# Kernel tuning notes

Measured on AMD Instinct MI355X. Metric: run time of the kernel, lower is better.

The kernel has to match this reference:

```python
import jax, jax.numpy as jnp
import numpy as np

D_MODEL = 1024
N_HEAD = 16
D_K = D_MODEL // N_HEAD
NEG = -1e9


def setup_inputs() -> dict:
    key = jax.random.key(0)
    ks = jax.random.split(key, 9)
    B, S = 2, 2048
    scale = 1.0 / np.sqrt(D_MODEL)
    x = jax.random.normal(ks[0], (B, S, D_MODEL), dtype=jnp.float32)
    mask = jnp.tril(jnp.ones((S, S), dtype=jnp.int32))  # causal: 0 => masked
    Wq = jax.random.normal(ks[1], (D_MODEL, D_MODEL), dtype=jnp.float32) * scale
    bq = jnp.zeros((D_MODEL,), dtype=jnp.float32)
    Wk = jax.random.normal(ks[2], (D_MODEL, D_MODEL), dtype=jnp.float32) * scale
    bk = jnp.zeros((D_MODEL,), dtype=jnp.float32)
    Wv = jax.random.normal(ks[3], (D_MODEL, D_MODEL), dtype=jnp.float32) * scale
    bv = jnp.zeros((D_MODEL,), dtype=jnp.float32)
    Wo = jax.random.normal(ks[4], (D_MODEL, D_MODEL), dtype=jnp.float32) * scale
    bo = jnp.zeros((D_MODEL,), dtype=jnp.float32)
    return {"x": x, "mask": mask, "Wq": Wq, "bq": bq, "Wk": Wk, "bk": bk,
            "Wv": Wv, "bv": bv, "Wo": Wo, "bo": bo}


def reference(x, mask, Wq, bq, Wk, bk, Wv, bv, Wo, bo):
    B, S, _ = x.shape
    # torch Linear: y = x @ W.T + b
    def split_heads(y):  # [B,S,D] -> [B,H,S,d_k]
        return y.reshape(B, S, N_HEAD, D_K).transpose(0, 2, 1, 3)
    Q = split_heads(x @ Wq.T + bq)
    K = split_heads(x @ Wk.T + bk)
    V = split_heads(x @ Wv.T + bv)
    scores = jnp.einsum('bhqd,bhkd->bhqk', Q, K) / jnp.sqrt(jnp.float32(D_K))
    scores = jnp.where(mask[None, None, :, :] == 0, jnp.float32(NEG), scores)
    attn = jax.nn.softmax(scores, axis=-1)
    out = jnp.einsum('bhqk,bhkd->bhqd', attn, V)
    out = out.transpose(0, 2, 1, 3).reshape(B, S, D_MODEL)
    return out @ Wo.T + bo
```

## Files before the change

### kernel.cpp

```cpp
#include <hip/hip_runtime.h>
#include <hip/hip_bf16.h>
#include <stdint.h>

#define DM    1024
#define NHEAD 16
#define DKH   64
#define SEQ   2048
#define NB    2
#define MTOT  (NB*SEQ)
#define LSTR  72
#define QSCL  0.18033688f

typedef __hip_bfloat16 bf16;
typedef __attribute__((ext_vector_type(8))) short bf16x8;
typedef __attribute__((ext_vector_type(4))) short bf16x4;
typedef __attribute__((ext_vector_type(4))) float f32x4;

#define MFMA16(a,b,c) __builtin_amdgcn_mfma_f32_16x16x32_bf16((a),(b),(c),0,0,0)

#if __has_builtin(__builtin_amdgcn_exp2f)
#define EXP2F(x) __builtin_amdgcn_exp2f(x)
#else
#define EXP2F(x) __expf(0.69314718056f * (x))
#endif

__device__ __forceinline__ void async_copy16(const void* g, void* l) {
  __builtin_amdgcn_global_load_lds((const __attribute__((address_space(1))) uint32_t*)g,
                                   (__attribute__((address_space(3))) uint32_t*)l,
                                   16, 0, 0);
}

__device__ __forceinline__ short f32_bf16_bits(float f) {
  uint32_t u = __builtin_bit_cast(uint32_t, f);
  u += 0x7FFFu + ((u >> 16) & 1u);
  return (short)(u >> 16);
}

__global__ __launch_bounds__(256) void k_cvt_all(
    const float* __restrict__ x,  const float* __restrict__ Wq,
    const float* __restrict__ Wk, const float* __restrict__ Wv,
    const float* __restrict__ Wo,
    bf16* __restrict__ xb,  bf16* __restrict__ Wqb, bf16* __restrict__ Wkb,
    bf16* __restrict__ Wvb, bf16* __restrict__ Wob) {
  const int NX = (MTOT*DM)/4;
  const int NW = (DM*DM)/4;
  int i = blockIdx.x * 256 + threadIdx.x;
  const float* s; bf16* d; int j; float scl = 1.0f;
  if (i < NX) { s = x; d = xb; j = i; }
  else {
    int t = i - NX;
    int k = t >> 18;
    j = t & (NW - 1);
    s = (k == 0) ? Wq : (k == 1) ? Wk : (k == 2) ? Wv : Wo;
    d = (k == 0) ? Wqb : (k == 1) ? Wkb : (k == 2) ? Wvb : Wob;
    if (k == 0) scl = QSCL;
  }
  float4 v = ((const float4*)s)[j];
  bf16x4 o;
  o[0] = f32_bf16_bits(v.x * scl);
  o[1] = f32_bf16_bits(v.y * scl);
  o[2] = f32_bf16_bits(v.z * scl);
  o[3] = f32_bf16_bits(v.w * scl);
  ((bf16x4*)d)[j] = o;
}

__global__ __launch_bounds__(256) void k_gemm_qkv(
    const bf16* __restrict__ x,
    const bf16* __restrict__ Wq, const bf16* __restrict__ Wk, const bf16* __restrict__ Wv,
    const float* __restrict__ bq, const float* __restrict__ bk, const float* __restrict__ bv,
    bf16* __restrict__ Q, bf16* __restrict__ K, bf16* __restrict__ V) {
  const int id  = blockIdx.x + (blockIdx.y << 5) + (blockIdx.z << 8);
  const int xcd = id & 7;
  const int jj  = id >> 3;
  const int bxi = (xcd << 2) | (jj & 3);
  const int rem = jj >> 2;
  const int byi = rem & 7;
  const int bzi = rem >> 3;

  const bf16* W; const float* bias; bf16* C; float bs;
  if (bzi == 0)      { W = Wq; bias = bq; C = Q; bs = QSCL; }
  else if (bzi == 1) { W = Wk; bias = bk; C = K; bs = 1.0f; }
  else               { W = Wv; bias = bv; C = V; bs = 1.0f; }

  __shared__ __align__(16) short As[128*32];
  __shared__ __align__(16) short Bs[128*32];
  const int tid  = threadIdx.x;
  const int lane = tid & 63;
  const int w    = tid >> 6;
  const int wm   = (w & 1) << 6;
  const int wn   = (w >> 1) << 6;
  const int bm   = bxi << 7;
  const int bn   = byi << 7;
  const int m16  = lane & 15;
  const int quad = lane >> 4;
  const int koff = quad << 3;
  const int c0   = (w << 7) | lane;

  f32x4 acc[4][4] = {};

  for (int k0 = 0; k0 < DM; k0 += 32) {
    __syncthreads();
#pragma unroll
    for (int it = 0; it < 2; ++it) {
      int c   = c0 + (it << 6);
      int row = c >> 2;
      int kc  = c & 3;
      async_copy16(x + (size_t)(bm + row) * DM + k0 + (kc << 3),
                   &As[(size_t)((w << 7) + (it << 6)) << 3]);
      async_copy16(W + (size_t)(bn + row) * DM + k0 + (kc << 3),
                   &Bs[(size_t)((w << 7) + (it << 6)) << 3]);
    }
    __syncthreads();

    bf16x8 af[4], bfv[4];
#pragma unroll
    for (int t = 0; t < 4; ++t)
      af[t]  = *(const bf16x8*)&As[(wm + t*16 + m16) * 32 + koff];
#pragma unroll
    for (int t = 0; t < 4; ++t)
      bfv[t] = *(const bf16x8*)&Bs[(wn + t*16 + m16) * 32 + koff];
#pragma unroll
    for (int i = 0; i < 4; ++i)
#pragma unroll
      for (int j = 0; j < 4; ++j)
        acc[i][j] = MFMA16(af[i], bfv[j], acc[i][j]);
  }

  const int crow0 = bm + wm + (quad << 2);
  const int ccol0 = bn + wn + m16;
#pragma unroll
  for (int j = 0; j < 4; ++j) {
    float bv = bias[ccol0 + j*16] * bs;
#pragma unroll
    for (int i = 0; i < 4; ++i)
#pragma unroll
      for (int r = 0; r < 4; ++r)
        C[(size_t)(crow0 + i*16 + r) * DM + ccol0 + j*16] =
            (bf16)(acc[i][j][r] + bv);
  }
}

__global__ __launch_bounds__(256) void k_gemm_o(
    const bf16* __restrict__ A, const bf16* __restrict__ W,
    const float* __restrict__ bias, float* __restrict__ C) {
  const int id  = blockIdx.x + (blockIdx.y << 5);
  const int xcd = id & 7;
  const int jj  = id >> 3;
  const int bxi = (xcd << 2) | (jj & 3);
  const int byi = jj >> 2;

  __shared__ __align__(16) short As[128*32];
  __shared__ __align__(16) short Bs[64*32];
  const int tid  = threadIdx.x;
  const int lane = tid & 63;
  const int w    = tid >> 6;
  const int wm   = (w & 1) << 6;
  const int wn   = (w >> 1) << 5;
  const int bm   = bxi << 7;
  const int bn   = byi << 6;
  const int m16  = lane & 15;
  const int quad = lane >> 4;
  const int koff = quad << 3;
  const int cA   = (w << 7) | lane;
  const int cB   = (w << 6) | lane;

  f32x4 acc[4][2] = {};

  for (int k0 = 0; k0 < DM; k0 += 32) {
    __syncthreads();
#pragma unroll
    for (int it = 0; it < 2; ++it) {
      int c   = cA + (it << 6);
      int row = c >> 2;
      int kc  = c & 3;
      async_copy16(A + (size_t)(bm + row) * DM + k0 + (kc << 3),
                   &As[(size_t)((w << 7) + (it << 6)) << 3]);
    }
    {
      int row = cB >> 2;
      int kc  = cB & 3;
      async_copy16(W + (size_t)(bn + row) * DM + k0 + (kc << 3),
                   &Bs[(size_t)(w << 6) << 3]);
    }
    __syncthreads();

    bf16x8 af[4], bfv[2];
#pragma unroll
    for (int t = 0; t < 4; ++t)
      af[t]  = *(const bf16x8*)&As[(wm + t*16 + m16) * 32 + koff];
#pragma unroll
    for (int t = 0; t < 2; ++t)
      bfv[t] = *(const bf16x8*)&Bs[(wn + t*16 + m16) * 32 + koff];
#pragma unroll
    for (int i = 0; i < 4; ++i)
#pragma unroll
      for (int j = 0; j < 2; ++j)
        acc[i][j] = MFMA16(af[i], bfv[j], acc[i][j]);
  }

  const int crow0 = bm + wm + (quad << 2);
  const int ccol0 = bn + wn + m16;
#pragma unroll
  for (int j = 0; j < 2; ++j) {
    float bv = bias[ccol0 + j*16];
#pragma unroll
    for (int i = 0; i < 4; ++i)
#pragma unroll
      for (int r = 0; r < 4; ++r)
        C[(size_t)(crow0 + i*16 + r) * DM + ccol0 + j*16] =
            acc[i][j][r] + bv;
  }
}

__global__ __launch_bounds__(256) void k_transpose_v(const bf16* __restrict__ V,
                                                     bf16* __restrict__ Vt) {
  __shared__ __align__(16) short tile[64][LSTR];
  const int tid = threadIdx.x;
  const int s0  = blockIdx.x << 6;
  const int bh  = blockIdx.y;
  const int b   = bh >> 4, h = bh & 15;
#pragma unroll
  for (int it = 0; it < 2; ++it) {
    int c = tid + (it << 8);
    int s = c >> 3, dc = c & 7;
    bf16x8 v = *(const bf16x8*)&V[(size_t)(b*SEQ + s0 + s) * DM + h*DKH + (dc << 3)];
    *(bf16x8*)&tile[s][dc << 3] = v;
  }
  __syncthreads();
#pragma unroll
  for (int it = 0; it < 2; ++it) {
    int c = tid + (it << 8);
    int d = c >> 3, sc = c & 7;
    bf16x8 ov;
#pragma unroll
    for (int i = 0; i < 8; ++i) {
      int p = (sc << 3) + i;
      ov[i] = tile[(p & 3) * 16 + (p >> 2)][d];
    }
    *(bf16x8*)&Vt[((size_t)bh * DKH + d) * SEQ + s0 + (sc << 3)] = ov;
  }
}

__global__ __launch_bounds__(256) void k_attn(const bf16* __restrict__ Q,
                                              const bf16* __restrict__ K,
                                              const bf16* __restrict__ Vt,
                                              bf16* __restrict__ ctx) {
  __shared__ __align__(16) short Ks[64*LSTR];
  __shared__ __align__(16) short Vs[64*LSTR];
  __shared__ __align__(16) short Ps[4][16*LSTR];

  const int tid  = threadIdx.x;
  const int lane = tid & 63;
  const int w    = tid >> 6;
  const int pi   = blockIdx.x;
  const int bh   = blockIdx.y;
  const int b    = bh >> 4, h = bh & 15;
  const int m16  = lane & 15, quad = lane >> 4;
  const int koff = quad << 3;

  const int qt        = (w < 2) ? pi : 63 - pi;
  const int qw        = (qt << 5) + ((w & 1) << 4);
  const int my_ktmax  = qt >> 1;
  const int blk_ktmax = (63 - pi) >> 1;

  const int r0 = tid >> 3, r1 = r0 + 32, c0 = (tid & 7) << 3;

  const bf16* Kb  = K  + (size_t)(b*SEQ) * DM + h*DKH;
  const bf16* Vtb = Vt + (size_t)bh * DKH * SEQ;

  const bf16* Qb = Q + (size_t)(b*SEQ + qw) * DM + h*DKH;
  bf16x8 qf0 = *(const bf16x8*)(Qb + (size_t)m16*DM + koff);
  bf16x8 qf1 = *(const bf16x8*)(Qb + (size_t)m16*DM + 32 + koff);

  f32x4 o[4] = {};
  float ps[4] = {0.f, 0.f, 0.f, 0.f};
  short* Pw = Ps[w];
  const int qg = qw + (quad << 2);

  bf16x8 pk0 = *(const bf16x8*)(Kb  + (size_t)r0*DM + c0);
  bf16x8 pk1 = *(const bf16x8*)(Kb  + (size_t)r1*DM + c0);
  bf16x8 pv0 = *(const bf16x8*)(Vtb + (size_t)r0*SEQ + c0);
  bf16x8 pv1 = *(const bf16x8*)(Vtb + (size_t)r1*SEQ + c0);

  for (int kt = 0; kt <= blk_ktmax; ++kt) {
    __syncthreads();
    *(bf16x8*)&Ks[r0*LSTR + c0] = pk0;
    *(bf16x8*)&Ks[r1*LSTR + c0] = pk1;
    *(bf16x8*)&Vs[r0*LSTR + c0] = pv0;
    *(bf16x8*)&Vs[r1*LSTR + c0] = pv1;
    __syncthreads();

    if (kt < blk_ktmax) {
      const int kn = (kt + 1) << 6;
      pk0 = *(const bf16x8*)(Kb  + (size_t)(kn + r0)*DM + c0);
      pk1 = *(const bf16x8*)(Kb  + (size_t)(kn + r1)*DM + c0);
      pv0 = *(const bf16x8*)(Vtb + (size_t)r0*SEQ + kn + c0);
      pv1 = *(const bf16x8*)(Vtb + (size_t)r1*SEQ + kn + c0);
    }

    if (kt <= my_ktmax) {
      f32x4 sc[4];
#pragma unroll
      for (int st = 0; st < 4; ++st) {
        bf16x8 kf0 = *(const bf16x8*)&Ks[(st*16 + m16)*LSTR + koff];
        bf16x8 kf1 = *(const bf16x8*)&Ks[(st*16 + m16)*LSTR + 32 + koff];
        f32x4 a = {};
        a = MFMA16(qf0, kf0, a);
        a = MFMA16(qf1, kf1, a);
        sc[st] = a;
      }
      const int kk0 = kt << 6;
      if (kt == my_ktmax) {
#pragma unroll
        for (int r = 0; r < 4; ++r) {
          float e[4];
#pragma unroll
          for (int st = 0; st < 4; ++st) {
            float t = EXP2F(sc[st][r]);
            t = (kk0 + st*16 + m16 <= qg + r) ? t : 0.f;
            e[st] = t; ps[r] += t;
          }
          uint32_t lo = (uint16_t)f32_bf16_bits(e[0]) |
                        ((uint32_t)(uint16_t)f32_bf16_bits(e[1]) << 16);
          uint32_t hi = (uint16_t)f32_bf16_bits(e[2]) |
                        ((uint32_t)(uint16_t)f32_bf16_bits(e[3]) << 16);
          *(uint64_t*)&Pw[((quad << 2) + r)*LSTR + (m16 << 2)] =
              (uint64_t)lo | ((uint64_t)hi << 32);
        }
      } else {
#pragma unroll
        for (int r = 0; r < 4; ++r) {
          float e[4];
#pragma unroll
          for (int st = 0; st < 4; ++st) {
            float t = EXP2F(sc[st][r]);
            e[st] = t; ps[r] += t;
          }
          uint32_t lo = (uint16_t)f32_bf16_bits(e[0]) |
                        ((uint32_t)(uint16_t)f32_bf16_bits(e[1]) << 16);
          uint32_t hi = (uint16_t)f32_bf16_bits(e[2]) |
                        ((uint32_t)(uint16_t)f32_bf16_bits(e[3]) << 16);
          *(uint64_t*)&Pw[((quad << 2) + r)*LSTR + (m16 << 2)] =
              (uint64_t)lo | ((uint64_t)hi << 32);
        }
      }
      asm volatile("s_waitcnt lgkmcnt(0)" ::: "memory");
      bf16x8 pa0 = *(const bf16x8*)&Pw[m16*LSTR + koff];
      bf16x8 pa1 = *(const bf16x8*)&Pw[m16*LSTR + 32 + koff];
#pragma unroll
      for (int t = 0; t < 4; ++t) {
        bf16x8 vf0 = *(const bf16x8*)&Vs[(t*16 + m16)*LSTR + koff];
        bf16x8 vf1 = *(const bf16x8*)&Vs[(t*16 + m16)*LSTR + 32 + koff];
        o[t] = MFMA16(pa0, vf0, o[t]);
        o[t] = MFMA16(pa1, vf1, o[t]);
      }
    }
  }

  bf16* Cb = ctx + (size_t)(b*SEQ + qw) * DM + h*DKH;
#pragma unroll
  for (int r = 0; r < 4; ++r) {
    float v = ps[r];
    v += __shfl_xor(v, 1, 64);
    v += __shfl_xor(v, 2, 64);
    v += __shfl_xor(v, 4, 64);
    v += __shfl_xor(v, 8, 64);
    float inv = 1.0f / v;
#pragma unroll
    for (int t = 0; t < 4; ++t)
      Cb[(size_t)((quad << 2) + r) * DM + t*16 + m16] = (bf16)(o[t][r] * inv);
  }
}

extern "C" void kernel_launch(void* const* d_in, const int* in_sizes, int n_in,
                              void* d_out, int out_size, void* d_ws, size_t ws_size,
                              hipStream_t stream) {
  const float* x  = (const float*)d_in[0];
  const float* Wq = (const float*)d_in[2];
  const float* bq = (const float*)d_in[3];
  const float* Wk = (const float*)d_in[4];
  const float* bk = (const float*)d_in[5];
  const float* Wv = (const float*)d_in[6];
  const float* bv = (const float*)d_in[7];
  const float* Wo = (const float*)d_in[8];
  const float* bo = (const float*)d_in[9];
  float* out = (float*)d_out;

  const size_t SZ = (size_t)MTOT * DM;
  const size_t WZ = (size_t)DM * DM;
  bf16* xb  = (bf16*)d_ws;
  bf16* Wqb = xb  + SZ;
  bf16* Wkb = Wqb + WZ;
  bf16* Wvb = Wkb + WZ;
  bf16* Wob = Wvb + WZ;
  bf16* Qb  = Wob + WZ;
  bf16* Kb  = Qb  + SZ;
  bf16* Vb  = Kb  + SZ;
  bf16* Vtb = Vb  + SZ;
  bf16* Cx  = xb;

  k_cvt_all<<<(SZ/4 + 4*(WZ/4))/256, 256, 0, stream>>>(
      x, Wq, Wk, Wv, Wo, xb, Wqb, Wkb, Wvb, Wob);

  k_gemm_qkv<<<dim3(MTOT/128, DM/128, 3), 256, 0, stream>>>(
      xb, Wqb, Wkb, Wvb, bq, bk, bv, Qb, Kb, Vb);
  k_transpose_v<<<dim3(SEQ/64, NB*NHEAD), 256, 0, stream>>>(Vb, Vtb);
  k_attn<<<dim3(32, NB*NHEAD), 256, 0, stream>>>(Qb, Kb, Vtb, Cx);
  k_gemm_o<<<dim3(MTOT/128, DM/64), 256, 0, stream>>>(Cx, Wob, bo, out);
}
```

Measured before the change: 203.0 us.

## Keep softmax probabilities in registers by computing transposed scores and permuting V

Computes S^T (K as the A operand) so each lane holds scores for one query row across keys, packs the exponentials with hardware bf16 pack instructions straight into the A-operand registers for the PV MFMA, and drops the per-wave LDS staging of P. The V transpose kernel permutes key order so the register layout of P matches V's k dimension. The row-sum reduction is rewritten around the new layout, and launch bounds request higher occupancy. This removes LDS writes, the reads back and a wait per tile, at the cost of a subtle layout coupling between kernels and switching bf16 rounding to the hardware convert.

```diff
diff --git a/kernel.cpp b/kernel.cpp
--- a/kernel.cpp
+++ b/kernel.cpp
@@ -15,6 +15,7 @@
 typedef __attribute__((ext_vector_type(8))) short bf16x8;
 typedef __attribute__((ext_vector_type(4))) short bf16x4;
 typedef __attribute__((ext_vector_type(4))) float f32x4;
+typedef __attribute__((ext_vector_type(4))) uint32_t u32x4;
 
 #define MFMA16(a,b,c) __builtin_amdgcn_mfma_f32_16x16x32_bf16((a),(b),(c),0,0,0)
 
@@ -34,6 +35,12 @@
   uint32_t u = __builtin_bit_cast(uint32_t, f);
   u += 0x7FFFu + ((u >> 16) & 1u);
   return (short)(u >> 16);
+}
+
+__device__ __forceinline__ uint32_t cvt_pk_bf16(float a, float b) {
+  uint32_t r;
+  asm("v_cvt_pk_bf16_f32 %0, %1, %2" : "=v"(r) : "v"(a), "v"(b));
+  return r;
 }
 
 __global__ __launch_bounds__(256) void k_cvt_all(
@@ -234,20 +241,22 @@
     bf16x8 ov;
 #pragma unroll
     for (int i = 0; i < 8; ++i) {
-      int p = (sc << 3) + i;
-      ov[i] = tile[(p & 3) * 16 + (p >> 2)][d];
+      int p  = (sc << 3) + i;
+      int r  = p & 3;
+      int st = ((p >> 5) & 1) | (((p >> 2) & 1) << 1);
+      int q2 = (p >> 3) & 3;
+      ov[i] = tile[st*16 + q2*4 + r][d];
     }
     *(bf16x8*)&Vt[((size_t)bh * DKH + d) * SEQ + s0 + (sc << 3)] = ov;
   }
 }
 
-__global__ __launch_bounds__(256) void k_attn(const bf16* __restrict__ Q,
-                                              const bf16* __restrict__ K,
-                                              const bf16* __restrict__ Vt,
-                                              bf16* __restrict__ ctx) {
+__global__ __launch_bounds__(256, 8) void k_attn(const bf16* __restrict__ Q,
+                                                 const bf16* __restrict__ K,
+                                                 const bf16* __restrict__ Vt,
+                                                 bf16* __restrict__ ctx) {
   __shared__ __align__(16) short Ks[64*LSTR];
   __shared__ __align__(16) short Vs[64*LSTR];
-  __shared__ __align__(16) short Ps[4][16*LSTR];
 
   const int tid  = threadIdx.x;
   const int lane = tid & 63;
@@ -273,9 +282,9 @@
   bf16x8 qf1 = *(const bf16x8*)(Qb + (size_t)m16*DM + 32 + koff);
 
   f32x4 o[4] = {};
-  float ps[4] = {0.f, 0.f, 0.f, 0.f};
-  short* Pw = Ps[w];
-  const int qg = qw + (quad << 2);
+  float psum = 0.f;
+  const int qrow  = qw + m16;
+  const int kquad = quad << 2;
 
   bf16x8 pk0 = *(const bf16x8*)(Kb  + (size_t)r0*DM + c0);
   bf16x8 pk1 = *(const bf16x8*)(Kb  + (size_t)r1*DM + c0);
@@ -299,54 +308,52 @@
     }
 
     if (kt <= my_ktmax) {
-      f32x4 sc[4];
-#pragma unroll
-      for (int st = 0; st < 4; ++st) {
-        bf16x8 kf0 = *(const bf16x8*)&Ks[(st*16 + m16)*LSTR + koff];
-        bf16x8 kf1 = *(const bf16x8*)&Ks[(st*16 + m16)*LSTR + 32 + koff];
-        f32x4 a = {};
-        a = MFMA16(qf0, kf0, a);
-        a = MFMA16(qf1, kf1, a);
-        sc[st] = a;
-      }
-      const int kk0 = kt << 6;
+      u32x4 p0, p1;
+      const int kbase = (kt << 6) + kquad;
       if (kt == my_ktmax) {
 #pragma unroll
-        for (int r = 0; r < 4; ++r) {
+        for (int st = 0; st < 4; ++st) {
+          bf16x8 kf0 = *(const bf16x8*)&Ks[(st*16 + m16)*LSTR + koff];
+          bf16x8 kf1 = *(const bf16x8*)&Ks[(st*16 + m16)*LSTR + 32 + koff];
+          f32x4 a = {};
+          a = MFMA16(kf0, qf0, a);
+          a = MFMA16(kf1, qf1, a);
           float e[4];
 #pragma unroll
-          for (int st = 0; st < 4; ++st) {
-            float t = EXP2F(sc[st][r]);
-            t = (kk0 + st*16 + m16 <= qg + r) ? t : 0.f;
-            e[st] = t; ps[r] += t;
+          for (int r = 0; r < 4; ++r) {
+            float t = EXP2F(a[r]);
+            t = (kbase + (st << 4) + r <= qrow) ? t : 0.f;
+            e[r] = t; psum += t;
           }
-          uint32_t lo = (uint16_t)f32_bf16_bits(e[0]) |
-                        ((uint32_t)(uint16_t)f32_bf16_bits(e[1]) << 16);
-          uint32_t hi = (uint16_t)f32_bf16_bits(e[2]) |
-                        ((uint32_t)(uint16_t)f32_bf16_bits(e[3]) << 16);
-          *(uint64_t*)&Pw[((quad << 2) + r)*LSTR + (m16 << 2)] =
-              (uint64_t)lo | ((uint64_t)hi << 32);
+          uint32_t lo = cvt_pk_bf16(e[0], e[1]);
+          uint32_t hi = cvt_pk_bf16(e[2], e[3]);
+          int base = st & 2;
+          if (st & 1) { p1[base] = lo; p1[base + 1] = hi; }
+          else        { p0[base] = lo; p0[base + 1] = hi; }
         }
       } else {
 #pragma unroll
-        for (int r = 0; r < 4; ++r) {
+        for (int st = 0; st < 4; ++st) {
+          bf16x8 kf0 = *(const bf16x8*)&Ks[(st*16 + m16)*LSTR + koff];
+          bf16x8 kf1 = *(const bf16x8*)&Ks[(st*16 + m16)*LSTR + 32 + koff];
+          f32x4 a = {};
+          a = MFMA16(kf0, qf0, a);
+          a = MFMA16(kf1, qf1, a);
           float e[4];
 #pragma unroll
-          for (int st = 0; st < 4; ++st) {
-            float t = EXP2F(sc[st][r]);
-            e[st] = t; ps[r] += t;
+          for (int r = 0; r < 4; ++r) {
+            float t = EXP2F(a[r]);
+            e[r] = t; psum += t;
           }
-          uint32_t lo = (uint16_t)f32_bf16_bits(e[0]) |
-                        ((uint32_t)(uint16_t)f32_bf16_bits(e[1]) << 16);
-          uint32_t hi = (uint16_t)f32_bf16_bits(e[2]) |
-                        ((uint32_t)(uint16_t)f32_bf16_bits(e[3]) << 16);
-          *(uint64_t*)&Pw[((quad << 2) + r)*LSTR + (m16 << 2)] =
-              (uint64_t)lo | ((uint64_t)hi << 32);
+          uint32_t lo = cvt_pk_bf16(e[0], e[1]);
+          uint32_t hi = cvt_pk_bf16(e[2], e[3]);
+          int base = st & 2;
+          if (st & 1) { p1[base] = lo; p1[base + 1] = hi; }
+          else        { p0[base] = lo; p0[base + 1] = hi; }
         }
       }
-      asm volatile("s_waitcnt lgkmcnt(0)" ::: "memory");
-      bf16x8 pa0 = *(const bf16x8*)&Pw[m16*LSTR + koff];
-      bf16x8 pa1 = *(const bf16x8*)&Pw[m16*LSTR + 32 + koff];
+      bf16x8 pa0 = __builtin_bit_cast(bf16x8, p0);
+      bf16x8 pa1 = __builtin_bit_cast(bf16x8, p1);
 #pragma unroll
       for (int t = 0; t < 4; ++t) {
         bf16x8 vf0 = *(const bf16x8*)&Vs[(t*16 + m16)*LSTR + koff];
@@ -357,18 +364,18 @@
     }
   }
 
+  float v = psum;
+  v += __shfl_xor(v, 16, 64);
+  v += __shfl_xor(v, 32, 64);
+  const int lanebase = lane & 48;
   bf16* Cb = ctx + (size_t)(b*SEQ + qw) * DM + h*DKH;
 #pragma unroll
   for (int r = 0; r < 4; ++r) {
-    float v = ps[r];
-    v += __shfl_xor(v, 1, 64);
-    v += __shfl_xor(v, 2, 64);
-    v += __shfl_xor(v, 4, 64);
-    v += __shfl_xor(v, 8, 64);
-    float inv = 1.0f / v;
+    float rs  = __shfl(v, lanebase | (kquad | r), 64);
+    float inv = 1.0f / rs;
 #pragma unroll
     for (int t = 0; t < 4; ++t)
-      Cb[(size_t)((quad << 2) + r) * DM + t*16 + m16] = (bf16)(o[t][r] * inv);
+      Cb[(size_t)(kquad + r) * DM + t*16 + m16] = (bf16)(o[t][r] * inv);
   }
 }
 
```

Result: slower. 215.3 us (+6.0%).

## Fuse V transpose into QKV GEMM epilogue, dropping the transpose kernel

Applied to the files above, without the earlier changes.

The V projection tile now writes its output straight into the transposed Vt layout inside the QKV GEMM epilogue, using bf16x4 stores along the sequence. The separate k_transpose_v kernel and its intermediate V buffer are removed. This saves one kernel launch and a full read and write of V through global memory. In exchange, the epilogue must produce the same permuted sequence order the attention kernel expects, and its stores are narrow and strided.

```diff
diff --git a/kernel.cpp b/kernel.cpp
--- a/kernel.cpp
+++ b/kernel.cpp
@@ -68,7 +68,7 @@
     const bf16* __restrict__ x,
     const bf16* __restrict__ Wq, const bf16* __restrict__ Wk, const bf16* __restrict__ Wv,
     const float* __restrict__ bq, const float* __restrict__ bk, const float* __restrict__ bv,
-    bf16* __restrict__ Q, bf16* __restrict__ K, bf16* __restrict__ V) {
+    bf16* __restrict__ Q, bf16* __restrict__ K, bf16* __restrict__ Vt) {
   const int id  = blockIdx.x + (blockIdx.y << 5) + (blockIdx.z << 8);
   const int xcd = id & 7;
   const int jj  = id >> 3;
@@ -77,10 +77,10 @@
   const int byi = rem & 7;
   const int bzi = rem >> 3;
 
-  const bf16* W; const float* bias; bf16* C; float bs;
-  if (bzi == 0)      { W = Wq; bias = bq; C = Q; bs = QSCL; }
-  else if (bzi == 1) { W = Wk; bias = bk; C = K; bs = 1.0f; }
-  else               { W = Wv; bias = bv; C = V; bs = 1.0f; }
+  const bf16* W; const float* bias; float bs;
+  if (bzi == 0)      { W = Wq; bias = bq; bs = QSCL; }
+  else if (bzi == 1) { W = Wk; bias = bk; bs = 1.0f; }
+  else               { W = Wv; bias = bv; bs = 1.0f; }
 
   __shared__ __align__(16) short As[128*32];
   __shared__ __align__(16) short Bs[128*32];
@@ -126,17 +126,41 @@
         acc[i][j] = MFMA16(af[i], bfv[j], acc[i][j]);
   }
 
-  const int crow0 = bm + wm + (quad << 2);
   const int ccol0 = bn + wn + m16;
-#pragma unroll
-  for (int j = 0; j < 4; ++j) {
-    float bv = bias[ccol0 + j*16] * bs;
-#pragma unroll
-    for (int i = 0; i < 4; ++i)
-#pragma unroll
-      for (int r = 0; r < 4; ++r)
-        C[(size_t)(crow0 + i*16 + r) * DM + ccol0 + j*16] =
-            (bf16)(acc[i][j][r] + bv);
+  if (bzi != 2) {
+    bf16* C = (bzi == 0) ? Q : K;
+    const int crow0 = bm + wm + (quad << 2);
+#pragma unroll
+    for (int j = 0; j < 4; ++j) {
+      float bvv = bias[ccol0 + j*16] * bs;
+#pragma unroll
+      for (int i = 0; i < 4; ++i)
+#pragma unroll
+        for (int r = 0; r < 4; ++r)
+          C[(size_t)(crow0 + i*16 + r) * DM + ccol0 + j*16] =
+              (bf16)(acc[i][j][r] + bvv);
+    }
+  } else {
+    const int brow  = bm + wm;
+    const int bloc  = brow >> 11;
+    const int sbase = brow & (SEQ - 1);
+    const int pr    = quad << 2;
+#pragma unroll
+    for (int j = 0; j < 4; ++j) {
+      int dg  = ccol0 + j*16;
+      int hh  = dg >> 6, dd = dg & 63;
+      int bhv = (bloc << 4) | hh;
+      float bvv = bias[dg];
+      bf16* dst = Vt + ((size_t)((bhv << 6) | dd)) * SEQ + sbase;
+#pragma unroll
+      for (int r = 0; r < 4; ++r) {
+        bf16x4 v4;
+#pragma unroll
+        for (int i = 0; i < 4; ++i)
+          v4[i] = f32_bf16_bits(acc[i][j][r] + bvv);
+        *(bf16x4*)&dst[(pr + r) << 2] = v4;
+      }
+    }
   }
 }
 
@@ -209,35 +233,6 @@
       for (int r = 0; r < 4; ++r)
         C[(size_t)(crow0 + i*16 + r) * DM + ccol0 + j*16] =
             acc[i][j][r] + bv;
-  }
-}
-
-__global__ __launch_bounds__(256) void k_transpose_v(const bf16* __restrict__ V,
-                                                     bf16* __restrict__ Vt) {
-  __shared__ __align__(16) short tile[64][LSTR];
-  const int tid = threadIdx.x;
-  const int s0  = blockIdx.x << 6;
-  const int bh  = blockIdx.y;
-  const int b   = bh >> 4, h = bh & 15;
-#pragma unroll
-  for (int it = 0; it < 2; ++it) {
-    int c = tid + (it << 8);
-    int s = c >> 3, dc = c & 7;
-    bf16x8 v = *(const bf16x8*)&V[(size_t)(b*SEQ + s0 + s) * DM + h*DKH + (dc << 3)];
-    *(bf16x8*)&tile[s][dc << 3] = v;
-  }
-  __syncthreads();
-#pragma unroll
-  for (int it = 0; it < 2; ++it) {
-    int c = tid + (it << 8);
-    int d = c >> 3, sc = c & 7;
-    bf16x8 ov;
-#pragma unroll
-    for (int i = 0; i < 8; ++i) {
-      int p = (sc << 3) + i;
-      ov[i] = tile[(p & 3) * 16 + (p >> 2)][d];
-    }
-    *(bf16x8*)&Vt[((size_t)bh * DKH + d) * SEQ + s0 + (sc << 3)] = ov;
   }
 }
 
@@ -395,16 +390,14 @@
   bf16* Wob = Wvb + WZ;
   bf16* Qb  = Wob + WZ;
   bf16* Kb  = Qb  + SZ;
-  bf16* Vb  = Kb  + SZ;
-  bf16* Vtb = Vb  + SZ;
+  bf16* Vtb = Kb  + SZ;
   bf16* Cx  = xb;
 
   k_cvt_all<<<(SZ/4 + 4*(WZ/4))/256, 256, 0, stream>>>(
       x, Wq, Wk, Wv, Wo, xb, Wqb, Wkb, Wvb, Wob);
 
   k_gemm_qkv<<<dim3(MTOT/128, DM/128, 3), 256, 0, stream>>>(
-      xb, Wqb, Wkb, Wvb, bq, bk, bv, Qb, Kb, Vb);
-  k_transpose_v<<<dim3(SEQ/64, NB*NHEAD), 256, 0, stream>>>(Vb, Vtb);
+      xb, Wqb, Wkb, Wvb, bq, bk, bv, Qb, Kb, Vtb);
   k_attn<<<dim3(32, NB*NHEAD), 256, 0, stream>>>(Qb, Kb, Vtb, Cx);
   k_gemm_o<<<dim3(MTOT/128, DM/64), 256, 0, stream>>>(Cx, Wob, bo, out);
 }
```

Result: slower. 211.6 us (+4.2%).
